# Kernel optimization log

Measured on AMD Instinct MI355X. Metric: run time of the kernel, lower is better.

## Reference

```python
import jax, jax.numpy as jnp
import numpy as np

DIM = 4096
N_HEADS = 32
HEAD_DIM = 128
N_KV_HEADS = 8
REPEAT = N_HEADS // N_KV_HEADS  # 4
B = 8
# ragged per-sequence lengths, fixed so total token count is static (jit-friendly)
SEQLEN = np.array([1024, 3072, 2048, 2560, 1536, 2048, 1792, 2304], dtype=np.int64)
TOTAL = int(SEQLEN.sum())  # 16384


def setup_inputs() -> dict:
    key = jax.random.key(0)
    k1, k2, k3 = jax.random.split(key, 3)
    embedding = jax.random.normal(k1, (B, DIM), dtype=jnp.float32)
    # nn.Linear weights: stored as [out_features, in_features]
    W_up = jax.random.normal(k2, (N_KV_HEADS * HEAD_DIM, DIM), dtype=jnp.float32) * (DIM ** -0.5)
    W_down = jax.random.normal(k3, (DIM, N_HEADS * HEAD_DIM), dtype=jnp.float32) * ((N_HEADS * HEAD_DIM) ** -0.5)
    seqlen = jnp.asarray(SEQLEN)
    return {"embedding": embedding, "W_up": W_up, "W_down": W_down, "seqlen": seqlen}


def reference(embedding, W_up, W_down, seqlen):
    # up-projection: [B, dim] -> [B, n_kv_heads*head_dim]
    x = embedding @ W_up.T
    # split kv heads and repeat-interleave to n_heads: [B, n_kv, hd] -> [B, n_heads, hd]
    xv = x.reshape(B, N_KV_HEADS, HEAD_DIM)
    val = jnp.repeat(xv, REPEAT, axis=1).reshape(B, N_HEADS * HEAD_DIM)  # [B, dim]
    # ragged broadcast: row i repeated seqlen[i] times -> [TOTAL, dim]
    out = jnp.repeat(val, seqlen, axis=0, total_repeat_length=TOTAL)
    # down-projection on every token row (redundant per-sequence math, as in original)
    return out @ W_down.T  # [TOTAL, dim]
```

## Files before the change

### kernel.cpp

```cpp
#include <hip/hip_runtime.h>

#define DIM   4096
#define NKV   8
#define HD    128
#define KVDIM 1024
#define NB    8
#define TOTAL 16384

__global__ __launch_bounds__(256)
void k_up(const float* __restrict__ emb, const float* __restrict__ wup,
          float* __restrict__ x) {
    int wid  = blockIdx.x * 4 + (threadIdx.x >> 6);
    int lane = threadIdx.x & 63;
    int j = wid >> 3;
    int b = wid & 7;
    const float4* e = (const float4*)(emb + b * DIM);
    const float4* w = (const float4*)(wup + (long)j * DIM);
    float acc = 0.f;
    #pragma unroll
    for (int it = lane; it < DIM / 4; it += 64) {
        float4 ev = e[it], wv = w[it];
        acc += ev.x * wv.x + ev.y * wv.y + ev.z * wv.z + ev.w * wv.w;
    }
    #pragma unroll
    for (int off = 32; off; off >>= 1) acc += __shfl_down(acc, off, 64);
    if (lane == 0) x[b * KVDIM + j] = acc;
}

__global__ __launch_bounds__(256)
void k_down(const float* __restrict__ x, const float* __restrict__ wdn,
            float* __restrict__ y) {
    int o    = blockIdx.x * 4 + (threadIdx.x >> 6);
    int lane = threadIdx.x & 63;
    const float4* w = (const float4*)(wdn + (long)o * DIM);
    float acc[NB];
    #pragma unroll
    for (int b = 0; b < NB; b++) acc[b] = 0.f;
    for (int it = lane; it < DIM / 4; it += 64) {
        int k0 = it * 4;
        int kv = ((k0 >> 9) << 7) + (k0 & 127);
        float4 wv = w[it];
        #pragma unroll
        for (int b = 0; b < NB; b++) {
            const float4 xv = *(const float4*)(x + b * KVDIM + kv);
            acc[b] += xv.x * wv.x + xv.y * wv.y + xv.z * wv.z + xv.w * wv.w;
        }
    }
    #pragma unroll
    for (int b = 0; b < NB; b++) {
        #pragma unroll
        for (int off = 32; off; off >>= 1) acc[b] += __shfl_down(acc[b], off, 64);
    }
    if (lane < NB) y[lane * DIM + o] = acc[lane];
}

__global__ __launch_bounds__(256)
void k_down_fix(const float* __restrict__ x, const float* __restrict__ wdn,
                float* __restrict__ y) {
    int o    = blockIdx.x * 4 + (threadIdx.x >> 6);
    int lane = threadIdx.x & 63;
    const float4* w = (const float4*)(wdn + (long)o * DIM);
    float acc[NB];
    #pragma unroll
    for (int b = 0; b < NB; b++) acc[b] = 0.f;
    for (int it = lane; it < DIM / 4; it += 64) {
        int k0 = it * 4;
        int kv = ((k0 >> 9) << 7) + (k0 & 127);
        float4 wv = w[it];
        #pragma unroll
        for (int b = 0; b < NB; b++) {
            const float4 xv = *(const float4*)(x + b * KVDIM + kv);
            acc[b] += xv.x * wv.x + xv.y * wv.y + xv.z * wv.z + xv.w * wv.w;
        }
    }
    #pragma unroll
    for (int b = 0; b < NB; b++) {
        #pragma unroll
        for (int off = 32; off; off >>= 1) acc[b] += __shfl_down(acc[b], off, 64);
        if (lane == 0) y[b * DIM + o] = acc[b];
    }
}

__global__ __launch_bounds__(256)
void k_bcast(const float* __restrict__ y, const int* __restrict__ seqlen,
             float4* __restrict__ out) {
    int row = blockIdx.x;
    int s = 0, acc = 0;
    #pragma unroll
    for (int i = 0; i < 7; i++) { acc += seqlen[i]; if (row >= acc) s = i + 1; }
    const float4* yr = (const float4*)(y + s * DIM);
    float4* orow = out + (long)row * (DIM / 4);
    #pragma unroll
    for (int c = threadIdx.x; c < DIM / 4; c += 256)
        orow[c] = yr[c];
}

extern "C" void kernel_launch(void* const* d_in, const int* in_sizes, int n_in,
                              void* d_out, int out_size, void* d_ws, size_t ws_size,
                              hipStream_t stream) {
    const float* emb = (const float*)d_in[0];
    const float* wup = (const float*)d_in[1];
    const float* wdn = (const float*)d_in[2];
    const int* seqlen = (const int*)d_in[3];

    float* x = (float*)d_ws;
    float* y = x + NB * KVDIM;

    k_up       <<<NB * KVDIM / 4, 256, 0, stream>>>(emb, wup, x);
    k_down_fix <<<DIM / 4,        256, 0, stream>>>(x, wdn, y);
    k_bcast    <<<TOTAL,          256, 0, stream>>>(y, seqlen, (float4*)d_out);
}
```

Measured before the change: 352.2 us.

## Fuse up, down and broadcast stages into one cooperative kernel with grid syncs

Replaces three separate kernel launches with a single cooperative kernel of 1024 blocks that runs the up-projection, the down-projection and the ragged broadcast, separated by grid-wide syncs. Each block loops over 16 output rows in the broadcast phase and writes them with nontemporal stores. The aim is to remove launch gaps between stages and reduce cache pollution from the 256 MB output write. The trade-offs are the cost of the grid syncs and lower parallelism in the broadcast phase, and the cooperative launch will fail if all 1024 blocks cannot be co-resident.

```diff
diff --git a/kernel.cpp b/kernel.cpp
--- a/kernel.cpp
+++ b/kernel.cpp
@@ -1,98 +1,92 @@
 #include <hip/hip_runtime.h>
+#include <hip/hip_cooperative_groups.h>
+
+namespace cg = cooperative_groups;
 
 #define DIM   4096
-#define NKV   8
-#define HD    128
 #define KVDIM 1024
 #define NB    8
 #define TOTAL 16384
+#define NBLK  1024
 
-__global__ __launch_bounds__(256)
-void k_up(const float* __restrict__ emb, const float* __restrict__ wup,
-          float* __restrict__ x) {
-    int wid  = blockIdx.x * 4 + (threadIdx.x >> 6);
-    int lane = threadIdx.x & 63;
-    int j = wid >> 3;
-    int b = wid & 7;
-    const float4* e = (const float4*)(emb + b * DIM);
-    const float4* w = (const float4*)(wup + (long)j * DIM);
-    float acc = 0.f;
+typedef float fvec4 __attribute__((ext_vector_type(4)));
+
+__global__ __launch_bounds__(256, 4)
+void fused_pca(const float* __restrict__ emb, const float* __restrict__ wup,
+               const float* __restrict__ wdn, const int* __restrict__ seqlen,
+               float* __restrict__ x, float* __restrict__ y,
+               float* __restrict__ out) {
+    cg::grid_group grid = cg::this_grid();
+    const int lane = threadIdx.x & 63;
+    const int wid  = blockIdx.x * 4 + (threadIdx.x >> 6);
+
     #pragma unroll
-    for (int it = lane; it < DIM / 4; it += 64) {
-        float4 ev = e[it], wv = w[it];
-        acc += ev.x * wv.x + ev.y * wv.y + ev.z * wv.z + ev.w * wv.w;
+    for (int i = 0; i < 2; i++) {
+        int d = wid * 2 + i;
+        int j = d >> 3;
+        int b = d & 7;
+        const fvec4* e = (const fvec4*)(emb + b * DIM);
+        const fvec4* w = (const fvec4*)(wup + (long)j * DIM);
+        float acc = 0.f;
+        #pragma unroll
+        for (int it = lane; it < DIM / 4; it += 64) {
+            fvec4 ev = e[it], wv = w[it];
+            fvec4 p = ev * wv;
+            acc += p.x + p.y + p.z + p.w;
+        }
+        #pragma unroll
+        for (int off = 32; off; off >>= 1) acc += __shfl_down(acc, off, 64);
+        if (lane == 0) x[b * KVDIM + j] = acc;
     }
-    #pragma unroll
-    for (int off = 32; off; off >>= 1) acc += __shfl_down(acc, off, 64);
-    if (lane == 0) x[b * KVDIM + j] = acc;
-}
 
-__global__ __launch_bounds__(256)
-void k_down(const float* __restrict__ x, const float* __restrict__ wdn,
-            float* __restrict__ y) {
-    int o    = blockIdx.x * 4 + (threadIdx.x >> 6);
-    int lane = threadIdx.x & 63;
-    const float4* w = (const float4*)(wdn + (long)o * DIM);
-    float acc[NB];
-    #pragma unroll
-    for (int b = 0; b < NB; b++) acc[b] = 0.f;
-    for (int it = lane; it < DIM / 4; it += 64) {
-        int k0 = it * 4;
-        int kv = ((k0 >> 9) << 7) + (k0 & 127);
-        float4 wv = w[it];
+    grid.sync();
+
+    {
+        int o = wid;
+        const fvec4* w = (const fvec4*)(wdn + (long)o * DIM);
+        float acc[NB];
+        #pragma unroll
+        for (int b = 0; b < NB; b++) acc[b] = 0.f;
+        for (int it = lane; it < DIM / 4; it += 64) {
+            int k0 = it * 4;
+            int kv = ((k0 >> 9) << 7) + (k0 & 127);
+            fvec4 wv = w[it];
+            #pragma unroll
+            for (int b = 0; b < NB; b++) {
+                const fvec4 xv = *(const fvec4*)(x + b * KVDIM + kv);
+                fvec4 p = xv * wv;
+                acc[b] += p.x + p.y + p.z + p.w;
+            }
+        }
         #pragma unroll
         for (int b = 0; b < NB; b++) {
-            const float4 xv = *(const float4*)(x + b * KVDIM + kv);
-            acc[b] += xv.x * wv.x + xv.y * wv.y + xv.z * wv.z + xv.w * wv.w;
+            #pragma unroll
+            for (int off = 32; off; off >>= 1) acc[b] += __shfl_down(acc[b], off, 64);
+            if (lane == 0) y[b * DIM + o] = acc[b];
         }
     }
-    #pragma unroll
-    for (int b = 0; b < NB; b++) {
+
+    grid.sync();
+
+    int c0 = seqlen[0];
+    int c1 = c0 + seqlen[1];
+    int c2 = c1 + seqlen[2];
+    int c3 = c2 + seqlen[3];
+    int c4 = c3 + seqlen[4];
+    int c5 = c4 + seqlen[5];
+    int c6 = c5 + seqlen[6];
+    for (int g = 0; g < TOTAL / NBLK; g++) {
+        int row = blockIdx.x + g * NBLK;
+        int s = (row >= c0) + (row >= c1) + (row >= c2) + (row >= c3)
+              + (row >= c4) + (row >= c5) + (row >= c6);
+        const fvec4* yr = (const fvec4*)(y + s * DIM);
+        fvec4* orow = (fvec4*)(out + (long)row * DIM);
         #pragma unroll
-        for (int off = 32; off; off >>= 1) acc[b] += __shfl_down(acc[b], off, 64);
-    }
-    if (lane < NB) y[lane * DIM + o] = acc[lane];
-}
-
-__global__ __launch_bounds__(256)
-void k_down_fix(const float* __restrict__ x, const float* __restrict__ wdn,
-                float* __restrict__ y) {
-    int o    = blockIdx.x * 4 + (threadIdx.x >> 6);
-    int lane = threadIdx.x & 63;
-    const float4* w = (const float4*)(wdn + (long)o * DIM);
-    float acc[NB];
-    #pragma unroll
-    for (int b = 0; b < NB; b++) acc[b] = 0.f;
-    for (int it = lane; it < DIM / 4; it += 64) {
-        int k0 = it * 4;
-        int kv = ((k0 >> 9) << 7) + (k0 & 127);
-        float4 wv = w[it];
-        #pragma unroll
-        for (int b = 0; b < NB; b++) {
-            const float4 xv = *(const float4*)(x + b * KVDIM + kv);
-            acc[b] += xv.x * wv.x + xv.y * wv.y + xv.z * wv.z + xv.w * wv.w;
+        for (int c = threadIdx.x; c < DIM / 4; c += 256) {
+            fvec4 v = yr[c];
+            __builtin_nontemporal_store(v, orow + c);
         }
     }
-    #pragma unroll
-    for (int b = 0; b < NB; b++) {
-        #pragma unroll
-        for (int off = 32; off; off >>= 1) acc[b] += __shfl_down(acc[b], off, 64);
-        if (lane == 0) y[b * DIM + o] = acc[b];
-    }
-}
-
-__global__ __launch_bounds__(256)
-void k_bcast(const float* __restrict__ y, const int* __restrict__ seqlen,
-             float4* __restrict__ out) {
-    int row = blockIdx.x;
-    int s = 0, acc = 0;
-    #pragma unroll
-    for (int i = 0; i < 7; i++) { acc += seqlen[i]; if (row >= acc) s = i + 1; }
-    const float4* yr = (const float4*)(y + s * DIM);
-    float4* orow = out + (long)row * (DIM / 4);
-    #pragma unroll
-    for (int c = threadIdx.x; c < DIM / 4; c += 256)
-        orow[c] = yr[c];
 }
 
 extern "C" void kernel_launch(void* const* d_in, const int* in_sizes, int n_in,
@@ -105,8 +99,10 @@
 
     float* x = (float*)d_ws;
     float* y = x + NB * KVDIM;
+    float* out = (float*)d_out;
 
-    k_up       <<<NB * KVDIM / 4, 256, 0, stream>>>(emb, wup, x);
-    k_down_fix <<<DIM / 4,        256, 0, stream>>>(x, wdn, y);
-    k_bcast    <<<TOTAL,          256, 0, stream>>>(y, seqlen, (float4*)d_out);
+    void* args[] = {(void*)&emb, (void*)&wup, (void*)&wdn, (void*)&seqlen,
+                    (void*)&x, (void*)&y, (void*)&out};
+    (void)hipLaunchCooperativeKernel((const void*)fused_pca, dim3(NBLK), dim3(256),
+                                     args, 0, stream);
 }
```

Result: slower. 516.4 us (+46.6%).
